# Optimization experiments

Hardware: AMD Instinct MI355X
Metric: run time of the kernel (lower is better)

## Reference

```python
import jax, jax.numpy as jnp
import numpy as np

HID = 256      # cfg.MODEL.YOSO.HIDDEN_DIM
NPROP = 100    # cfg.MODEL.YOSO.NUM_PROPOSALS
K1 = 3         # CONV_KERNEL_SIZE_1D
K2 = 1         # CONV_KERNEL_SIZE_2D
NCLS = 80      # NUM_CLASSES
NHEAD = 8

def layernorm(x, g, b, eps=1e-5):
    m = jnp.mean(x, -1, keepdims=True)
    v = jnp.var(x, -1, keepdims=True)
    return (x - m) * jax.lax.rsqrt(v + eps) * g + b

def dysep(query, value, Wl, bl, ng, nb):
    # dynamic depthwise conv (kernel K1 along feature axis, one kernel per proposal)
    # followed by dynamic pointwise NxN conv, per torch F.conv1d semantics (cross-correlation, 'same' pad)
    w = query @ Wl + bl                      # [B,N,N+K1]
    dw = w[..., :K1]                         # [B,N,K1] depthwise kernels
    pw = w[..., K1:]                         # [B,N,N]  pointwise mixing
    C = value.shape[-1]
    pad = K1 // 2
    vp = jnp.pad(value, ((0, 0), (0, 0), (pad, pad)))
    depth = sum(dw[..., k:k + 1] * vp[..., k:k + C] for k in range(K1))
    depth = jax.nn.relu(depth)
    point = jnp.einsum('bmn,bnc->bmc', pw, depth)
    return layernorm(point, ng, nb)

def mha(x, in_w, in_b, out_w, out_b):
    B, N, E = x.shape
    d = E // NHEAD
    qkv = x @ in_w + in_b
    q, k, v = jnp.split(qkv, 3, axis=-1)
    q = q.reshape(B, N, NHEAD, d)
    k = k.reshape(B, N, NHEAD, d)
    v = v.reshape(B, N, NHEAD, d)
    att = jnp.einsum('bqhd,bkhd->bhqk', q, k) / jnp.sqrt(jnp.asarray(d, x.dtype))
    att = jax.nn.softmax(att, axis=-1)
    o = jnp.einsum('bhqk,bkhd->bqhd', att, v).reshape(B, N, E)
    return o @ out_w + out_b

def setup_inputs() -> dict:
    key = jax.random.key(0)
    ks = iter(jax.random.split(key, 64))
    B, H, W = 8, 128, 128
    E = HID * K2 * K2
    nrm = lambda *s: jax.random.normal(next(ks), s, jnp.float32) * 0.02
    bias_value = -np.log((1 - 0.01) / 0.01)
    return dict(
        features=jax.random.normal(next(ks), (B, HID, H, W), jnp.float32),
        proposal_kernels=jax.random.normal(next(ks), (B, NPROP, E), jnp.float32),
        mask_preds=jax.random.normal(next(ks), (B, NPROP, H, W), jnp.float32),
        fW=nrm(E, NPROP + K1), fb=jnp.zeros(NPROP + K1), fng=jnp.ones(E), fnb=jnp.zeros(E),
        f_norm_g=jnp.ones(E), f_norm_b=jnp.zeros(E),
        kW=nrm(E, NPROP + K1), kb=jnp.zeros(NPROP + K1), kng=jnp.ones(E), knb=jnp.zeros(E),
        k_norm_g=jnp.ones(E), k_norm_b=jnp.zeros(E),
        attn_in_w=nrm(E, 3 * E), attn_in_b=jnp.zeros(3 * E),
        attn_out_w=nrm(E, E), attn_out_b=jnp.zeros(E),
        s_norm_g=jnp.ones(E), s_norm_b=jnp.zeros(E),
        ffn_w1=nrm(HID, 2048), ffn_b1=jnp.zeros(2048),
        ffn_w2=nrm(2048, HID), ffn_b2=jnp.zeros(HID),
        ffn_norm_g=jnp.ones(HID), ffn_norm_b=jnp.zeros(HID),
        cls_w=nrm(HID, HID), cls_ln_g=jnp.ones(HID), cls_ln_b=jnp.zeros(HID),
        fc_cls_w=nrm(HID, NCLS + 1), fc_cls_b=jnp.full((NCLS + 1,), bias_value, jnp.float32),
        mask_w=nrm(3, HID, HID), mask_ln_g=jnp.ones((3, HID)), mask_ln_b=jnp.zeros((3, HID)),
        fc_mask_w=nrm(HID, HID), fc_mask_b=jnp.zeros(HID),
        train_flag=1,
    )

def reference(features, proposal_kernels, mask_preds, fW, fb, fng, fnb, f_norm_g, f_norm_b,
              kW, kb, kng, knb, k_norm_g, k_norm_b,
              attn_in_w, attn_in_b, attn_out_w, attn_out_b, s_norm_g, s_norm_b,
              ffn_w1, ffn_b1, ffn_w2, ffn_b2, ffn_norm_g, ffn_norm_b,
              cls_w, cls_ln_g, cls_ln_b, fc_cls_w, fc_cls_b,
              mask_w, mask_ln_g, mask_ln_b, fc_mask_w, fc_mask_b, train_flag):
    B, C, H, W = features.shape
    hard = (jax.nn.sigmoid(mask_preds) > 0.5).astype(features.dtype)   # hard masks (no grad path)
    f = jnp.einsum('bnhw,bchw->bnc', hard, features)                   # mask-pooled features [B,N,E]
    k = proposal_kernels.reshape(B, NPROP, -1)
    f = layernorm(f + dysep(k, f, fW, fb, fng, fnb), f_norm_g, f_norm_b)
    kk = layernorm(f + dysep(k, f, kW, kb, kng, knb), k_norm_g, k_norm_b)
    kk = layernorm(kk + mha(kk, attn_in_w, attn_in_b, attn_out_w, attn_out_b), s_norm_g, s_norm_b)
    obj = jnp.transpose(kk.reshape(B, NPROP, HID, -1), (0, 1, 3, 2))   # [B,N,K2*K2,HID]
    h = jax.nn.relu(obj @ ffn_w1 + ffn_b1)
    obj = layernorm(obj + (h @ ffn_w2 + ffn_b2), ffn_norm_g, ffn_norm_b)
    cls_feat = obj.sum(-2)                                             # [B,N,HID]
    mask_feat = obj
    if train_flag:
        cls_feat = jax.nn.relu(layernorm(cls_feat @ cls_w, cls_ln_g, cls_ln_b))
        cls_score = (cls_feat @ fc_cls_w + fc_cls_b).reshape(B, NPROP, -1)
    else:
        cls_score = None
    for i in range(mask_w.shape[0]):
        mask_feat = jax.nn.relu(layernorm(mask_feat @ mask_w[i], mask_ln_g[i], mask_ln_b[i]))
    mask_kernels = (mask_feat @ fc_mask_w + fc_mask_b)[:, :, 0, :]     # squeeze(2), K2*K2==1
    new_mask_preds = jnp.einsum('bqc,bchw->bqhw', mask_kernels, features)
    obj_out = jnp.transpose(obj, (0, 1, 3, 2)).reshape(B, NPROP, HID, K2, K2)
    return (cls_score, new_mask_preds, obj_out)
```

## Files before the change

### kernel.cpp

```cpp
#include <hip/hip_runtime.h>

typedef float f32x4 __attribute__((ext_vector_type(4)));
typedef short bfrag __attribute__((ext_vector_type(8)));
typedef short sh4 __attribute__((ext_vector_type(4)));

__device__ __forceinline__ unsigned short f2bf(float x) {
  unsigned int u = __float_as_uint(x);
  return (unsigned short)((u + 0x7FFFu + ((u >> 16) & 1u)) >> 16);
}
__device__ __forceinline__ float bf2f(unsigned short u) {
  return __uint_as_float(((unsigned int)u) << 16);
}
__device__ __forceinline__ float wred_sum(float v) {
#pragma unroll
  for (int o = 32; o > 0; o >>= 1) v += __shfl_xor(v, o);
  return v;
}
__device__ __forceinline__ float wred_max(float v) {
#pragma unroll
  for (int o = 32; o > 0; o >>= 1) v = fmaxf(v, __shfl_xor(v, o));
  return v;
}

struct Prep6 {
  const float* s[6];
  int K[6];
  int N[6];
  int base[6];
  int doff[6];
};

__global__ __launch_bounds__(256) void prep_w(Prep6 p, unsigned short* wt) {
  int t = blockIdx.x;
  int wi = 0;
#pragma unroll
  for (int i = 0; i < 5; ++i)
    if (t >= p.base[i + 1]) wi = i + 1;
  int lt = t - p.base[wi];
  int K = p.K[wi], N = p.N[wi];
  int tkn = (K + 31) >> 5;
  int tk = lt % tkn, tn = lt / tkn;
  __shared__ float tile[32][33];
  const float* src = p.s[wi];
#pragma unroll
  for (int i = 0; i < 4; ++i) {
    int flat = i * 256 + threadIdx.x;
    int kl = flat >> 5, nl = flat & 31;
    int k = tk * 32 + kl, n = tn * 32 + nl;
    tile[kl][nl] = (k < K && n < N) ? src[(size_t)k * N + n] : 0.f;
  }
  __syncthreads();
  unsigned short* dst = wt + p.doff[wi];
#pragma unroll
  for (int i = 0; i < 4; ++i) {
    int flat = i * 256 + threadIdx.x;
    int nl = flat >> 5, kl = flat & 31;
    int k = tk * 32 + kl, n = tn * 32 + nl;
    if (k < K && n < N) {
      int np = (wi < 2) ? ((n >= 3) ? n - 3 : n + 100) : n;
      dst[(size_t)np * K + k] = f2bf(tile[kl][nl]);
    }
  }
}

__global__ __launch_bounds__(256) void prep_bias(const float* __restrict__ fb_,
                                                 const float* __restrict__ kb_,
                                                 float* __restrict__ bfk) {
  int t = threadIdx.x;
  if (t < 103) {
    int np = (t >= 3) ? t - 3 : t + 100;
    bfk[np] = fb_[t];
    bfk[104 + np] = kb_[t];
  }
  if (t == 103) { bfk[103] = 0.f; bfk[207] = 0.f; }
}

struct Cast4 {
  const float* s[4];
  int n[4];
  int base[4];
  int doff[4];
};

__global__ __launch_bounds__(256) void cast_w(Cast4 cc, unsigned short* dst) {
  int t = blockIdx.x;
  int wi = 0;
#pragma unroll
  for (int i = 0; i < 3; ++i)
    if (t >= cc.base[i + 1]) wi = i + 1;
  int lt = t - cc.base[wi];
  int idx = lt * 1024 + threadIdx.x * 4;
  if (idx + 3 < cc.n[wi]) {
    float4 v = *(const float4*)(cc.s[wi] + idx);
    sh4 o;
    o[0] = (short)f2bf(v.x); o[1] = (short)f2bf(v.y);
    o[2] = (short)f2bf(v.z); o[3] = (short)f2bf(v.w);
    *(sh4*)(dst + cc.doff[wi] + idx) = o;
  }
}

__global__ __launch_bounds__(256) void pack_bits(const float* __restrict__ mask,
                                                 unsigned int* __restrict__ bits) {
  int tid = threadIdx.x;
  size_t f = (size_t)blockIdx.x * 256 + tid;
  float4 m = *(const float4*)(mask + f * 4);
  unsigned int n = (m.x > 0.f ? 1u : 0u) | (m.y > 0.f ? 2u : 0u) |
                   (m.z > 0.f ? 4u : 0u) | (m.w > 0.f ? 8u : 0u);
  n <<= ((tid & 7) * 4);
  n |= (unsigned int)__shfl_xor((int)n, 1);
  n |= (unsigned int)__shfl_xor((int)n, 2);
  n |= (unsigned int)__shfl_xor((int)n, 4);
  if ((tid & 7) == 0) bits[((size_t)blockIdx.x * 32) + (tid >> 3)] = n;
}

template <int ABF, int OBF>
__global__ __launch_bounds__(256) void gemm_mf(const void* Av,
                                               const unsigned short* __restrict__ Wt,
                                               const float* __restrict__ bias,
                                               void* Cv, int M, int K, int N, int ldc, int relu,
                                               int kspan) {
  __shared__ short Al[64 * 72];
  __shared__ short Wl[64 * 72];
  int tid = threadIdx.x;
  int r0 = blockIdx.x * 64;
  int c0 = blockIdx.y * 64;
  int kz = blockIdx.z * kspan;
  int w = tid >> 6, lane = tid & 63, quad = lane >> 4, l15 = lane & 15;

  f32x4 acc[4];
#pragma unroll
  for (int mt = 0; mt < 4; ++mt) {
    acc[mt][0] = 0.f; acc[mt][1] = 0.f; acc[mt][2] = 0.f; acc[mt][3] = 0.f;
  }

  for (int k0 = kz; k0 < kz + kspan; k0 += 64) {
    if (ABF) {
      const unsigned short* A = (const unsigned short*)Av;
#pragma unroll
      for (int p = 0; p < 2; ++p) {
        int flat = p * 256 + tid;
        int row = flat >> 3, k8 = flat & 7;
        bfrag v;
        if (r0 + row < M)
          v = *(const bfrag*)(A + (size_t)(r0 + row) * K + k0 + k8 * 8);
        else
          v = (bfrag)(short)0;
        *(bfrag*)(Al + row * 72 + k8 * 8) = v;
      }
    } else {
      const float* A = (const float*)Av;
#pragma unroll
      for (int p = 0; p < 4; ++p) {
        int flat = p * 256 + tid;
        int row = flat >> 4, c4 = flat & 15;
        sh4 o4;
        if (r0 + row < M) {
          float4 v = *(const float4*)(A + (size_t)(r0 + row) * K + k0 + c4 * 4);
          o4[0] = (short)f2bf(v.x); o4[1] = (short)f2bf(v.y);
          o4[2] = (short)f2bf(v.z); o4[3] = (short)f2bf(v.w);
        } else {
          o4[0] = 0; o4[1] = 0; o4[2] = 0; o4[3] = 0;
        }
        *(sh4*)(Al + row * 72 + c4 * 4) = o4;
      }
    }
#pragma unroll
    for (int p = 0; p < 2; ++p) {
      int flat = p * 256 + tid;
      int row = flat >> 3, k8 = flat & 7;
      bfrag v;
      if (c0 + row < N)
        v = *(const bfrag*)(Wt + (size_t)(c0 + row) * K + k0 + k8 * 8);
      else
        v = (bfrag)(short)0;
      *(bfrag*)(Wl + row * 72 + k8 * 8) = v;
    }
    __syncthreads();
#pragma unroll
    for (int kk = 0; kk < 2; ++kk) {
      bfrag bv = *(const bfrag*)(Wl + (w * 16 + l15) * 72 + kk * 32 + quad * 8);
#pragma unroll
      for (int mt = 0; mt < 4; ++mt) {
        bfrag av = *(const bfrag*)(Al + (mt * 16 + l15) * 72 + kk * 32 + quad * 8);
        acc[mt] = __builtin_amdgcn_mfma_f32_16x16x32_bf16(av, bv, acc[mt], 0, 0, 0);
      }
    }
    __syncthreads();
  }
  int col = c0 + w * 16 + l15;
  if (col < N) {
    float bv = bias ? bias[col] : 0.f;
    size_t zoff = (size_t)blockIdx.z * M * ldc;
#pragma unroll
    for (int mt = 0; mt < 4; ++mt)
#pragma unroll
      for (int r = 0; r < 4; ++r) {
        int m = r0 + mt * 16 + quad * 4 + r;
        if (m < M) {
          float v = acc[mt][r] + bv;
          if (relu) v = fmaxf(v, 0.f);
          if (OBF)
            ((unsigned short*)Cv)[zoff + (size_t)m * ldc + col] = f2bf(v);
          else
            ((float*)Cv)[zoff + (size_t)m * ldc + col] = v;
        }
      }
  }
}

__global__ __launch_bounds__(512, 4) void phaseA(const unsigned int* __restrict__ bits,
                                                 const float* __restrict__ feat,
                                                 float* __restrict__ partial) {
  int tid = threadIdx.x;
  int ks = blockIdx.x;
  int ct = blockIdx.y;
  int b  = blockIdx.z;
  __shared__ short Al[2][112 * 72];
  __shared__ short Bl[2][128 * 72];
  int w = tid >> 6, lane = tid & 63, quad = lane >> 4, l15 = lane & 15;

  int rbase = tid >> 4;
  int c4 = tid & 15;
  const float* frow = feat + (size_t)(b * 256 + ct * 128 + rbase) * 16384 + c4 * 4;

  int arow = tid >> 2, q = tid & 3;
  bool aact = tid < 400;
  const unsigned int* brow = bits + (size_t)(b * 100 + arow) * 512 + (q >> 1);

  f32x4 acc[7];
#pragma unroll
  for (int mt = 0; mt < 7; ++mt) {
    acc[mt][0] = 0.f; acc[mt][1] = 0.f; acc[mt][2] = 0.f; acc[mt][3] = 0.f;
  }

  for (int z = tid; z < 384; z += 512) {
    int bufi = z / 192, rem = z % 192;
    sh4 zz; zz[0] = 0; zz[1] = 0; zz[2] = 0; zz[3] = 0;
    *(sh4*)(&Al[bufi][(100 + (rem >> 4)) * 72 + (rem & 15) * 4]) = zz;
  }

  int k0 = ks * 512;
  {
    float4 bpf[4];
    unsigned int awd = 0;
#pragma unroll
    for (int p = 0; p < 4; ++p)
      bpf[p] = *(const float4*)(frow + (size_t)p * 32 * 16384 + k0);
    if (aact) awd = brow[k0 >> 5];
#pragma unroll
    for (int p = 0; p < 4; ++p) {
      int row = rbase + 32 * p;
      sh4 o4b;
      o4b[0] = (short)f2bf(bpf[p].x);
      o4b[1] = (short)f2bf(bpf[p].y);
      o4b[2] = (short)f2bf(bpf[p].z);
      o4b[3] = (short)f2bf(bpf[p].w);
      *(sh4*)(&Bl[0][row * 72 + c4 * 4]) = o4b;
    }
    if (aact) {
      unsigned int hw16 = (awd >> ((q & 1) * 16)) & 0xFFFFu;
      bfrag e0, e1;
#pragma unroll
      for (int i = 0; i < 8; ++i) e0[i] = ((hw16 >> i) & 1u) ? (short)0x3F80 : (short)0;
#pragma unroll
      for (int i = 0; i < 8; ++i) e1[i] = ((hw16 >> (i + 8)) & 1u) ? (short)0x3F80 : (short)0;
      *(bfrag*)(&Al[0][arow * 72 + q * 16]) = e0;
      *(bfrag*)(&Al[0][arow * 72 + q * 16 + 8]) = e1;
    }
  }
  __syncthreads();

  int cur = 0;
  for (int st = 0; st < 8; ++st) {
    float4 bpf[4];
    unsigned int awd = 0;
    if (st < 7) {
      int kb = k0 + (st + 1) * 64;
#pragma unroll
      for (int p = 0; p < 4; ++p)
        bpf[p] = *(const float4*)(frow + (size_t)p * 32 * 16384 + kb);
      if (aact) awd = brow[kb >> 5];
    }
#pragma unroll
    for (int kk = 0; kk < 2; ++kk) {
      bfrag bv = *(const bfrag*)(&Bl[cur][(w * 16 + l15) * 72 + kk * 32 + quad * 8]);
#pragma unroll
      for (int mt = 0; mt < 7; ++mt) {
        bfrag av = *(const bfrag*)(&Al[cur][(mt * 16 + l15) * 72 + kk * 32 + quad * 8]);
        acc[mt] = __builtin_amdgcn_mfma_f32_16x16x32_bf16(av, bv, acc[mt], 0, 0, 0);
      }
    }
    __builtin_amdgcn_sched_barrier(0);
    if (st < 7) {
      int nxt = cur ^ 1;
#pragma unroll
      for (int p = 0; p < 4; ++p) {
        int row = rbase + 32 * p;
        sh4 o4b;
        o4b[0] = (short)f2bf(bpf[p].x);
        o4b[1] = (short)f2bf(bpf[p].y);
        o4b[2] = (short)f2bf(bpf[p].z);
        o4b[3] = (short)f2bf(bpf[p].w);
        *(sh4*)(&Bl[nxt][row * 72 + c4 * 4]) = o4b;
      }
      if (aact) {
        unsigned int hw16 = (awd >> ((q & 1) * 16)) & 0xFFFFu;
        bfrag e0, e1;
#pragma unroll
        for (int i = 0; i < 8; ++i) e0[i] = ((hw16 >> i) & 1u) ? (short)0x3F80 : (short)0;
#pragma unroll
        for (int i = 0; i < 8; ++i) e1[i] = ((hw16 >> (i + 8)) & 1u) ? (short)0x3F80 : (short)0;
        *(bfrag*)(&Al[nxt][arow * 72 + q * 16]) = e0;
        *(bfrag*)(&Al[nxt][arow * 72 + q * 16 + 8]) = e1;
      }
    }
    __syncthreads();
    cur ^= 1;
  }

  float* pb = partial + (size_t)(b * 32 + ks) * (100 * 256) + ct * 128 + w * 16 + l15;
#pragma unroll
  for (int mt = 0; mt < 7; ++mt)
#pragma unroll
    for (int r = 0; r < 4; ++r) {
      int m = mt * 16 + quad * 4 + r;
      if (m < 100) pb[(size_t)m * 256] = acc[mt][r];
    }
}

__global__ __launch_bounds__(256) void reduceA(const float* __restrict__ partial,
                                               float* __restrict__ fm) {
  int gid = blockIdx.x * 256 + threadIdx.x;
  int c = gid & 255, row = gid >> 8;
  int b = row / 100, n = row % 100;
  float s = 0.f;
#pragma unroll
  for (int ks = 0; ks < 32; ++ks)
    s += partial[((size_t)(b * 32 + ks) * 100 + n) * 256 + c];
  fm[(size_t)row * 256 + c] = s;
}

__global__ __launch_bounds__(256) void pointdw(const float* __restrict__ fm,
                                               const float* __restrict__ wbuf,
                                               float* __restrict__ point) {
  int tid = threadIdx.x;
  int b = blockIdx.y, c0 = blockIdx.x * 32;
  __shared__ float dl[100 * 33];
  for (int flat = tid; flat < 3200; flat += 256) {
    int n = flat >> 5, cl = flat & 31, c = c0 + cl;
    const float* fr = fm + (size_t)(b * 100 + n) * 256;
    const float* wr = wbuf + (size_t)(b * 100 + n) * 208;
    float x0 = (c > 0) ? fr[c - 1] : 0.f;
    float x1 = fr[c];
    float x2 = (c < 255) ? fr[c + 1] : 0.f;
    float d = wr[100] * x0 + wr[101] * x1 + wr[102] * x2;
    dl[n * 33 + cl] = fmaxf(d, 0.f);
  }
  __syncthreads();
  int cl = tid & 31, mg = tid >> 5;
  for (int m = mg; m < 100; m += 8) {
    const float4* pw4 = (const float4*)(wbuf + (size_t)(b * 100 + m) * 208);
    float a = 0.f;
#pragma unroll
    for (int n4 = 0; n4 < 25; ++n4) {
      float4 wv = pw4[n4];
      a += wv.x * dl[(n4 * 4 + 0) * 33 + cl] + wv.y * dl[(n4 * 4 + 1) * 33 + cl]
         + wv.z * dl[(n4 * 4 + 2) * 33 + cl] + wv.w * dl[(n4 * 4 + 3) * 33 + cl];
    }
    point[(size_t)(b * 100 + m) * 256 + c0 + cl] = a;
  }
}

__global__ __launch_bounds__(256) void ln2_kernel(const float* __restrict__ x,
                                                  const float* __restrict__ resid,
                                                  const float* __restrict__ g1, const float* __restrict__ b1,
                                                  const float* __restrict__ g2, const float* __restrict__ b2,
                                                  float* __restrict__ out) {
  int tid = threadIdx.x;
  int row = blockIdx.x * 4 + (tid >> 6);
  int lane = tid & 63;
  size_t base = (size_t)row * 256 + lane * 4;
  float4 v = *(const float4*)(x + base);
  float mean = wred_sum(v.x + v.y + v.z + v.w) * (1.f / 256.f);
  float d0 = v.x - mean, d1 = v.y - mean, d2 = v.z - mean, d3 = v.w - mean;
  float rs = rsqrtf(wred_sum(d0 * d0 + d1 * d1 + d2 * d2 + d3 * d3) * (1.f / 256.f) + 1e-5f);
  float4 gv = *(const float4*)(g1 + lane * 4);
  float4 bv = *(const float4*)(b1 + lane * 4);
  float4 rv = *(const float4*)(resid + base);
  float y0 = rv.x + d0 * rs * gv.x + bv.x;
  float y1 = rv.y + d1 * rs * gv.y + bv.y;
  float y2 = rv.z + d2 * rs * gv.z + bv.z;
  float y3 = rv.w + d3 * rs * gv.w + bv.w;
  float mean2 = wred_sum(y0 + y1 + y2 + y3) * (1.f / 256.f);
  float e0 = y0 - mean2, e1 = y1 - mean2, e2 = y2 - mean2, e3 = y3 - mean2;
  float rs2 = rsqrtf(wred_sum(e0 * e0 + e1 * e1 + e2 * e2 + e3 * e3) * (1.f / 256.f) + 1e-5f);
  float4 g2v = *(const float4*)(g2 + lane * 4);
  float4 b2v = *(const float4*)(b2 + lane * 4);
  float4 o;
  o.x = e0 * rs2 * g2v.x + b2v.x;
  o.y = e1 * rs2 * g2v.y + b2v.y;
  o.z = e2 * rs2 * g2v.z + b2v.z;
  o.w = e3 * rs2 * g2v.w + b2v.w;
  *(float4*)(out + base) = o;
}

__global__ __launch_bounds__(256) void ln_kernel(const float* __restrict__ x,
                                                 const float* __restrict__ res,
                                                 const float* __restrict__ g, const float* __restrict__ bb,
                                                 float* __restrict__ out, int relu,
                                                 float* __restrict__ copy2) {
  int tid = threadIdx.x;
  int row = blockIdx.x * 4 + (tid >> 6);
  int lane = tid & 63;
  size_t base = (size_t)row * 256 + lane * 4;
  float4 v = *(const float4*)(x + base);
  if (res) {
    float4 rv = *(const float4*)(res + base);
    v.x += rv.x; v.y += rv.y; v.z += rv.z; v.w += rv.w;
  }
  float mean = wred_sum(v.x + v.y + v.z + v.w) * (1.f / 256.f);
  float d0 = v.x - mean, d1 = v.y - mean, d2 = v.z - mean, d3 = v.w - mean;
  float rs = rsqrtf(wred_sum(d0 * d0 + d1 * d1 + d2 * d2 + d3 * d3) * (1.f / 256.f) + 1e-5f);
  float4 gv = *(const float4*)(g + lane * 4);
  float4 bv = *(const float4*)(bb + lane * 4);
  float4 o;
  o.x = d0 * rs * gv.x + bv.x;
  o.y = d1 * rs * gv.y + bv.y;
  o.z = d2 * rs * gv.z + bv.z;
  o.w = d3 * rs * gv.w + bv.w;
  if (relu) {
    o.x = fmaxf(o.x, 0.f); o.y = fmaxf(o.y, 0.f);
    o.z = fmaxf(o.z, 0.f); o.w = fmaxf(o.w, 0.f);
  }
  *(float4*)(out + base) = o;
  if (copy2) *(float4*)(copy2 + base) = o;
}

__global__ __launch_bounds__(256) void ln_ffn2(const float* __restrict__ t1,
                                               const float* __restrict__ b2,
                                               const float* __restrict__ res,
                                               const float* __restrict__ g, const float* __restrict__ bb,
                                               float* __restrict__ out,
                                               float* __restrict__ copy2) {
  int tid = threadIdx.x;
  int row = blockIdx.x * 4 + (tid >> 6);
  int lane = tid & 63;
  size_t base = (size_t)row * 256 + lane * 4;
  float4 v = *(const float4*)(t1 + base);
#pragma unroll
  for (int s = 1; s < 4; ++s) {
    float4 p = *(const float4*)(t1 + (size_t)s * 204800 + base);
    v.x += p.x; v.y += p.y; v.z += p.z; v.w += p.w;
  }
  float4 b2v = *(const float4*)(b2 + lane * 4);
  float4 rv = *(const float4*)(res + base);
  v.x += b2v.x + rv.x; v.y += b2v.y + rv.y; v.z += b2v.z + rv.z; v.w += b2v.w + rv.w;
  float mean = wred_sum(v.x + v.y + v.z + v.w) * (1.f / 256.f);
  float d0 = v.x - mean, d1 = v.y - mean, d2 = v.z - mean, d3 = v.w - mean;
  float rs = rsqrtf(wred_sum(d0 * d0 + d1 * d1 + d2 * d2 + d3 * d3) * (1.f / 256.f) + 1e-5f);
  float4 gv = *(const float4*)(g + lane * 4);
  float4 bv = *(const float4*)(bb + lane * 4);
  float4 o;
  o.x = d0 * rs * gv.x + bv.x;
  o.y = d1 * rs * gv.y + bv.y;
  o.z = d2 * rs * gv.z + bv.z;
  o.w = d3 * rs * gv.w + bv.w;
  *(float4*)(out + base) = o;
  *(float4*)(copy2 + base) = o;
}

__global__ __launch_bounds__(256) void attn_kernel(const float* __restrict__ qkv,
                                                   float* __restrict__ obuf) {
  int tid = threadIdx.x;
  int b = blockIdx.y, h = blockIdx.x & 7, qq = blockIdx.x >> 3;
  __shared__ float ktj[100 * 32];
  __shared__ unsigned short vl[100 * 32];
  __shared__ float sl[25 * 100];
  const float* base = qkv + (size_t)b * 100 * 768;
  for (int flat = tid; flat < 3200; flat += 256) {
    int j = flat >> 5, dd = flat & 31;
    ktj[j * 32 + dd] = base[(size_t)j * 768 + 256 + h * 32 + dd];
    vl[j * 32 + dd] = f2bf(base[(size_t)j * 768 + 512 + h * 32 + dd]);
  }
  __syncthreads();
  {
    int il = tid % 25;
    int jseg = tid / 25;
    int i = qq * 25 + il;
    const float4* q4 = (const float4*)(base + (size_t)i * 768 + h * 32);
    float4 q[8];
#pragma unroll
    for (int d4 = 0; d4 < 8; ++d4) q[d4] = q4[d4];
    if (jseg < 10) {
      for (int jj = 0; jj < 10; ++jj) {
        int j = jseg * 10 + jj;
        const float4* kr = (const float4*)(ktj + j * 32);
        float a = 0.f;
#pragma unroll
        for (int d4 = 0; d4 < 8; ++d4) {
          float4 kv = kr[d4];
          a += q[d4].x * kv.x + q[d4].y * kv.y + q[d4].z * kv.z + q[d4].w * kv.w;
        }
        sl[il * 100 + j] = a * 0.17677669529663687f;
      }
    }
  }
  __syncthreads();
  int w = tid >> 6, lane = tid & 63;
  for (int r = w; r < 25; r += 4) {
    float x0 = sl[r * 100 + lane];
    float x1 = (lane + 64 < 100) ? sl[r * 100 + lane + 64] : -1e30f;
    float mx = wred_max(fmaxf(x0, x1));
    float e0 = __expf(x0 - mx);
    float e1 = (lane + 64 < 100) ? __expf(x1 - mx) : 0.f;
    float inv = 1.f / wred_sum(e0 + e1);
    sl[r * 100 + lane] = e0 * inv;
    if (lane + 64 < 100) sl[r * 100 + lane + 64] = e1 * inv;
  }
  __syncthreads();
  for (int flat = tid; flat < 800; flat += 256) {
    int il = flat >> 5, dd = flat & 31;
    float a = 0.f;
#pragma unroll 4
    for (int j = 0; j < 100; ++j) a += sl[il * 100 + j] * bf2f(vl[j * 32 + dd]);
    obuf[(size_t)(b * 100 + qq * 25 + il) * 256 + h * 32 + dd] = a;
  }
}

__global__ __launch_bounds__(256) void head_fused(
    const float* __restrict__ objb,
    const unsigned short* __restrict__ whd,
    const float* __restrict__ cls_g, const float* __restrict__ cls_b,
    const float* __restrict__ fcclsb,
    const float* __restrict__ mask_g, const float* __restrict__ mask_b,
    const float* __restrict__ fcmb,
    float* __restrict__ out_cls, unsigned short* __restrict__ mk16) {
  const int WH_CLS = 0, WH_FCCLS = 65536, WH_M = 86272, WH_FCM = 282880;
  int tid = threadIdx.x, wv = tid >> 6, lane = tid & 63;
  int row = blockIdx.x;
  __shared__ float xs[256];
  __shared__ float x0s[256];
  __shared__ float ps[4][256];
  if (wv == 0) {
    float4 v = *(const float4*)(objb + (size_t)row * 256 + lane * 4);
    *(float4*)(&xs[lane * 4]) = v;
    *(float4*)(&x0s[lane * 4]) = v;
  }
  __syncthreads();
  int c = lane * 4;
  int kb = wv * 64;

  for (int li = 0; li < 3; ++li) {
    const unsigned short* W = whd + WH_M + li * 65536;
    float a0 = 0.f, a1 = 0.f, a2 = 0.f, a3 = 0.f;
#pragma unroll 8
    for (int k = kb; k < kb + 64; ++k) {
      float xk = xs[k];
      sh4 w4 = *(const sh4*)(W + (size_t)k * 256 + c);
      a0 += xk * bf2f((unsigned short)w4[0]);
      a1 += xk * bf2f((unsigned short)w4[1]);
      a2 += xk * bf2f((unsigned short)w4[2]);
      a3 += xk * bf2f((unsigned short)w4[3]);
    }
    ps[wv][c] = a0; ps[wv][c + 1] = a1; ps[wv][c + 2] = a2; ps[wv][c + 3] = a3;
    __syncthreads();
    float s0 = ps[0][c] + ps[1][c] + ps[2][c] + ps[3][c];
    float s1 = ps[0][c + 1] + ps[1][c + 1] + ps[2][c + 1] + ps[3][c + 1];
    float s2 = ps[0][c + 2] + ps[1][c + 2] + ps[2][c + 2] + ps[3][c + 2];
    float s3 = ps[0][c + 3] + ps[1][c + 3] + ps[2][c + 3] + ps[3][c + 3];
    float mean = wred_sum(s0 + s1 + s2 + s3) * (1.f / 256.f);
    float d0 = s0 - mean, d1 = s1 - mean, d2 = s2 - mean, d3 = s3 - mean;
    float rs = rsqrtf(wred_sum(d0 * d0 + d1 * d1 + d2 * d2 + d3 * d3) * (1.f / 256.f) + 1e-5f);
    float4 gv = *(const float4*)(mask_g + li * 256 + c);
    float4 bv = *(const float4*)(mask_b + li * 256 + c);
    float4 o;
    o.x = fmaxf(d0 * rs * gv.x + bv.x, 0.f);
    o.y = fmaxf(d1 * rs * gv.y + bv.y, 0.f);
    o.z = fmaxf(d2 * rs * gv.z + bv.z, 0.f);
    o.w = fmaxf(d3 * rs * gv.w + bv.w, 0.f);
    __syncthreads();
    *(float4*)(&xs[c]) = o;
    __syncthreads();
  }
  {
    const unsigned short* W = whd + WH_FCM;
    float a0 = 0.f, a1 = 0.f, a2 = 0.f, a3 = 0.f;
#pragma unroll 8
    for (int k = kb; k < kb + 64; ++k) {
      float xk = xs[k];
      sh4 w4 = *(const sh4*)(W + (size_t)k * 256 + c);
      a0 += xk * bf2f((unsigned short)w4[0]);
      a1 += xk * bf2f((unsigned short)w4[1]);
      a2 += xk * bf2f((unsigned short)w4[2]);
      a3 += xk * bf2f((unsigned short)w4[3]);
    }
    ps[wv][c] = a0; ps[wv][c + 1] = a1; ps[wv][c + 2] = a2; ps[wv][c + 3] = a3;
    __syncthreads();
    if (wv == 0) {
      float s0 = ps[0][c] + ps[1][c] + ps[2][c] + ps[3][c];
      float s1 = ps[0][c + 1] + ps[1][c + 1] + ps[2][c + 1] + ps[3][c + 1];
      float s2 = ps[0][c + 2] + ps[1][c + 2] + ps[2][c + 2] + ps[3][c + 2];
      float s3 = ps[0][c + 3] + ps[1][c + 3] + ps[2][c + 3] + ps[3][c + 3];
      float4 bv = *(const float4*)(fcmb + c);
      sh4 o;
      o[0] = (short)f2bf(s0 + bv.x); o[1] = (short)f2bf(s1 + bv.y);
      o[2] = (short)f2bf(s2 + bv.z); o[3] = (short)f2bf(s3 + bv.w);
      *(sh4*)(mk16 + (size_t)row * 256 + c) = o;
    }
    __syncthreads();
  }
  {
    const unsigned short* W = whd + WH_CLS;
    float a0 = 0.f, a1 = 0.f, a2 = 0.f, a3 = 0.f;
#pragma unroll 8
    for (int k = kb; k < kb + 64; ++k) {
      float xk = x0s[k];
      sh4 w4 = *(const sh4*)(W + (size_t)k * 256 + c);
      a0 += xk * bf2f((unsigned short)w4[0]);
      a1 += xk * bf2f((unsigned short)w4[1]);
      a2 += xk * bf2f((unsigned short)w4[2]);
      a3 += xk * bf2f((unsigned short)w4[3]);
    }
    ps[wv][c] = a0; ps[wv][c + 1] = a1; ps[wv][c + 2] = a2; ps[wv][c + 3] = a3;
    __syncthreads();
    float s0 = ps[0][c] + ps[1][c] + ps[2][c] + ps[3][c];
    float s1 = ps[0][c + 1] + ps[1][c + 1] + ps[2][c + 1] + ps[3][c + 1];
    float s2 = ps[0][c + 2] + ps[1][c + 2] + ps[2][c + 2] + ps[3][c + 2];
    float s3 = ps[0][c + 3] + ps[1][c + 3] + ps[2][c + 3] + ps[3][c + 3];
    float mean = wred_sum(s0 + s1 + s2 + s3) * (1.f / 256.f);
    float d0 = s0 - mean, d1 = s1 - mean, d2 = s2 - mean, d3 = s3 - mean;
    float rs = rsqrtf(wred_sum(d0 * d0 + d1 * d1 + d2 * d2 + d3 * d3) * (1.f / 256.f) + 1e-5f);
    float4 gv = *(const float4*)(cls_g + c);
    float4 bv = *(const float4*)(cls_b + c);
    float4 o;
    o.x = fmaxf(d0 * rs * gv.x + bv.x, 0.f);
    o.y = fmaxf(d1 * rs * gv.y + bv.y, 0.f);
    o.z = fmaxf(d2 * rs * gv.z + bv.z, 0.f);
    o.w = fmaxf(d3 * rs * gv.w + bv.w, 0.f);
    __syncthreads();
    *(float4*)(&xs[c]) = o;
    __syncthreads();
  }
  {
    const unsigned short* W = whd + WH_FCCLS;
    float a0 = 0.f, a1 = 0.f;
#pragma unroll 8
    for (int k = kb; k < kb + 64; ++k) {
      float xk = xs[k];
      a0 += xk * bf2f(W[(size_t)k * 81 + lane]);
      if (lane < 17) a1 += xk * bf2f(W[(size_t)k * 81 + 64 + lane]);
    }
    ps[wv][lane] = a0;
    if (lane < 17) ps[wv][64 + lane] = a1;
    __syncthreads();
    if (wv == 0) {
      float s = ps[0][lane] + ps[1][lane] + ps[2][lane] + ps[3][lane];
      out_cls[(size_t)row * 81 + lane] = s + fcclsb[lane];
      if (lane < 17) {
        float s2 = ps[0][64 + lane] + ps[1][64 + lane] + ps[2][64 + lane] + ps[3][64 + lane];
        out_cls[(size_t)row * 81 + 64 + lane] = s2 + fcclsb[64 + lane];
      }
    }
  }
}

__global__ __launch_bounds__(256, 4) void phaseE(const unsigned short* __restrict__ mk16,
                                                 const float* __restrict__ feat,
                                                 float* __restrict__ out) {
  int tid = threadIdx.x;
  int b = blockIdx.y;
  int hw0 = blockIdx.x * 128;
  int w = tid >> 6, lane = tid & 63, quad = lane >> 4, l15 = lane & 15;
  f32x4 acc[7][2];
#pragma unroll
  for (int mt = 0; mt < 7; ++mt)
#pragma unroll
    for (int nt = 0; nt < 2; ++nt) {
      acc[mt][nt][0] = 0.f; acc[mt][nt][1] = 0.f; acc[mt][nt][2] = 0.f; acc[mt][nt][3] = 0.f;
    }
  size_t fb = (size_t)b * 256 * 16384;
  int hwl = hw0 + w * 32 + l15;
  const unsigned short* mkb_b = mk16 + (size_t)b * 100 * 256;
  for (int kk = 0; kk < 8; ++kk) {
    bfrag bv[2];
#pragma unroll
    for (int nt = 0; nt < 2; ++nt) {
#pragma unroll
      for (int j = 0; j < 8; ++j) {
        float v = feat[fb + (size_t)(kk * 32 + quad * 8 + j) * 16384 + hwl + nt * 16];
        bv[nt][j] = (short)f2bf(v);
      }
    }
    bfrag av[7];
#pragma unroll
    for (int mt = 0; mt < 7; ++mt) {
      int row = mt * 16 + l15;
      int rr = (row < 100) ? row : 0;
      av[mt] = *(const bfrag*)(mkb_b + (size_t)rr * 256 + kk * 32 + quad * 8);
    }
#pragma unroll
    for (int mt = 0; mt < 7; ++mt) {
      acc[mt][0] = __builtin_amdgcn_mfma_f32_16x16x32_bf16(av[mt], bv[0], acc[mt][0], 0, 0, 0);
      acc[mt][1] = __builtin_amdgcn_mfma_f32_16x16x32_bf16(av[mt], bv[1], acc[mt][1], 0, 0, 0);
    }
  }
#pragma unroll
  for (int mt = 0; mt < 7; ++mt)
#pragma unroll
    for (int nt = 0; nt < 2; ++nt)
#pragma unroll
      for (int r = 0; r < 4; ++r) {
        int m = mt * 16 + quad * 4 + r;
        if (m < 100)
          out[(size_t)(b * 100 + m) * 16384 + hw0 + w * 32 + nt * 16 + l15] = acc[mt][nt][r];
      }
}

extern "C" void kernel_launch(void* const* d_in, const int* in_sizes, int n_in,
                              void* d_out, int out_size, void* d_ws, size_t ws_size,
                              hipStream_t stream) {
  const float* feat    = (const float*)d_in[0];
  const float* prop    = (const float*)d_in[1];
  const float* maskp   = (const float*)d_in[2];
  const float* fW      = (const float*)d_in[3];
  const float* fb_     = (const float*)d_in[4];
  const float* fng     = (const float*)d_in[5];
  const float* fnb     = (const float*)d_in[6];
  const float* f_ng    = (const float*)d_in[7];
  const float* f_nb    = (const float*)d_in[8];
  const float* kW      = (const float*)d_in[9];
  const float* kb_     = (const float*)d_in[10];
  const float* kng     = (const float*)d_in[11];
  const float* knb     = (const float*)d_in[12];
  const float* k_ng    = (const float*)d_in[13];
  const float* k_nb    = (const float*)d_in[14];
  const float* aw_in   = (const float*)d_in[15];
  const float* ab_in   = (const float*)d_in[16];
  const float* aw_out  = (const float*)d_in[17];
  const float* ab_out  = (const float*)d_in[18];
  const float* s_ng    = (const float*)d_in[19];
  const float* s_nb    = (const float*)d_in[20];
  const float* w1      = (const float*)d_in[21];
  const float* b1      = (const float*)d_in[22];
  const float* w2      = (const float*)d_in[23];
  const float* b2      = (const float*)d_in[24];
  const float* ffn_ng  = (const float*)d_in[25];
  const float* ffn_nb  = (const float*)d_in[26];
  const float* cls_w   = (const float*)d_in[27];
  const float* cls_g   = (const float*)d_in[28];
  const float* cls_b   = (const float*)d_in[29];
  const float* fcclsw  = (const float*)d_in[30];
  const float* fcclsb  = (const float*)d_in[31];
  const float* mask_w  = (const float*)d_in[32];
  const float* mask_g  = (const float*)d_in[33];
  const float* mask_b  = (const float*)d_in[34];
  const float* fcmw    = (const float*)d_in[35];
  const float* fcmb    = (const float*)d_in[36];
  float* out = (float*)d_out;

  float* ws = (float*)d_ws;
  size_t off = 0;
  unsigned short* wt = (unsigned short*)(ws + off); off += 681984;
  float* fm      = ws + off; off += 204800;
  float* bias_fk = ws + off; off += 208;
  unsigned int* bitsbuf = (unsigned int*)(ws + off); off += 409600;
  unsigned short* whd = (unsigned short*)(ws + off); off += 174208;
  float* partial = ws + off;
  float* ub = partial;
  size_t uo = 0;
  float* wb   = ub + uo; uo += 166400;
  float* pt   = ub + uo; uo += 204800;
  float* fbuf = ub + uo; uo += 204800;
  float* kkb  = ub + uo; uo += 204800;
  float* qkvb = ub + uo; uo += 614400;
  float* ob   = ub + uo; uo += 204800;
  float* mo   = ub + uo; uo += 204800;
  float* kk2  = ub + uo; uo += 204800;
  float* t1   = ub + uo; uo += 819200;
  float* objb = ub + uo; uo += 204800;
  float* mkb  = ub + uo; uo += 204800;
  unsigned short* ffn1b = (unsigned short*)(ub + uo); uo += 409600;
  unsigned short* mkb16 = (unsigned short*)mkb;

  const int wt_fW = 0, wt_kW = 26624, wt_ain = 53248, wt_aout = 249856;
  const int wt_w1 = 315392, wt_w2 = 839680;

  float* out_cls  = out;
  float* out_mask = out + 64800;
  float* out_obj  = out + 64800 + 13107200;

  Prep6 p;
  const float* srcs[6] = {fW, kW, aw_in, aw_out, w1, w2};
  int Ks[6]    = {256, 256, 256, 256, 256, 2048};
  int Ns[6]    = {103, 103, 768, 256, 2048, 256};
  int doffs[6] = {wt_fW, wt_kW, wt_ain, wt_aout, wt_w1, wt_w2};
  int tb = 0;
  for (int i = 0; i < 6; ++i) {
    p.s[i] = srcs[i]; p.K[i] = Ks[i]; p.N[i] = Ns[i]; p.doff[i] = doffs[i];
    p.base[i] = tb;
    tb += ((Ks[i] + 31) / 32) * ((Ns[i] + 31) / 32);
  }
  prep_w<<<tb, 256, 0, stream>>>(p, wt);
  prep_bias<<<1, 256, 0, stream>>>(fb_, kb_, bias_fk);
  Cast4 cc;
  const float* csrc[4] = {cls_w, fcclsw, mask_w, fcmw};
  int cn[4] = {65536, 20736, 196608, 65536};
  int cdoff[4] = {0, 65536, 86272, 282880};
  int cb = 0;
  for (int i = 0; i < 4; ++i) {
    cc.s[i] = csrc[i]; cc.n[i] = cn[i]; cc.doff[i] = cdoff[i];
    cc.base[i] = cb;
    cb += (cn[i] + 1023) / 1024;
  }
  cast_w<<<cb, 256, 0, stream>>>(cc, whd);
  pack_bits<<<12800, 256, 0, stream>>>(maskp, bitsbuf);

  phaseA<<<dim3(32, 2, 8), 512, 0, stream>>>(bitsbuf, feat, partial);
  reduceA<<<800, 256, 0, stream>>>(partial, fm);
  gemm_mf<0, 0><<<dim3(13, 4, 1), 256, 0, stream>>>(prop, wt + wt_fW, bias_fk, wb, 800, 256, 208, 208, 0, 256);
  pointdw<<<dim3(8, 8), 256, 0, stream>>>(fm, wb, pt);
  ln2_kernel<<<200, 256, 0, stream>>>(pt, fm, fng, fnb, f_ng, f_nb, fbuf);
  pointdw<<<dim3(8, 8), 256, 0, stream>>>(fbuf, wb + 104, pt);
  ln2_kernel<<<200, 256, 0, stream>>>(pt, fbuf, kng, knb, k_ng, k_nb, kkb);
  gemm_mf<0, 0><<<dim3(13, 12, 1), 256, 0, stream>>>(kkb, wt + wt_ain, ab_in, qkvb, 800, 256, 768, 768, 0, 256);
  attn_kernel<<<dim3(32, 8), 256, 0, stream>>>(qkvb, ob);
  gemm_mf<0, 0><<<dim3(13, 4, 1), 256, 0, stream>>>(ob, wt + wt_aout, ab_out, mo, 800, 256, 256, 256, 0, 256);
  ln_kernel<<<200, 256, 0, stream>>>(mo, kkb, s_ng, s_nb, kk2, 0, nullptr);
  gemm_mf<0, 1><<<dim3(13, 32, 1), 256, 0, stream>>>(kk2, wt + wt_w1, b1, ffn1b, 800, 256, 2048, 2048, 1, 256);
  gemm_mf<1, 0><<<dim3(13, 4, 4), 256, 0, stream>>>(ffn1b, wt + wt_w2, nullptr, t1, 800, 2048, 256, 256, 0, 512);
  ln_ffn2<<<200, 256, 0, stream>>>(t1, b2, kk2, ffn_ng, ffn_nb, objb, out_obj);
  head_fused<<<800, 256, 0, stream>>>(objb, whd, cls_g, cls_b, fcclsb,
                                      mask_g, mask_b, fcmb, out_cls, mkb16);
  phaseE<<<dim3(128, 8), 256, 0, stream>>>(mkb16, feat, out_mask);
}
```

Before: 588.0 us.

## Shrink phaseA channel tile to 64 and drop double buffering; widen pointdw grid

phaseA now uses 256-thread blocks covering 64 feature channels instead of 512 threads over 128. It drops the LDS double buffer in favour of a single-buffered load, sync, compute loop, and the grid doubles in channel tiles. The goal is more blocks and higher occupancy from smaller LDS use, since the kernel is bound by streaming the features. The cost is no overlap between global loads and MFMA within a block, with the mask-bit A tile rebuilt per block and twice as many blocks doing it. pointdw also halves its channel tile to 16 to launch twice as many blocks.

```diff
diff --git a/kernel.cpp b/kernel.cpp
--- a/kernel.cpp
+++ b/kernel.cpp
@@ -208,24 +208,23 @@
   }
 }
 
-__global__ __launch_bounds__(512, 4) void phaseA(const unsigned int* __restrict__ bits,
+__global__ __launch_bounds__(256, 6) void phaseA(const unsigned int* __restrict__ bits,
                                                  const float* __restrict__ feat,
                                                  float* __restrict__ partial) {
   int tid = threadIdx.x;
   int ks = blockIdx.x;
   int ct = blockIdx.y;
   int b  = blockIdx.z;
-  __shared__ short Al[2][112 * 72];
-  __shared__ short Bl[2][128 * 72];
+  __shared__ short Al[112 * 72];
+  __shared__ short Bl[64 * 72];
   int w = tid >> 6, lane = tid & 63, quad = lane >> 4, l15 = lane & 15;
 
-  int rbase = tid >> 4;
-  int c4 = tid & 15;
-  const float* frow = feat + (size_t)(b * 256 + ct * 128 + rbase) * 16384 + c4 * 4;
-
-  int arow = tid >> 2, q = tid & 3;
-  bool aact = tid < 400;
-  const unsigned int* brow = bits + (size_t)(b * 100 + arow) * 512 + (q >> 1);
+  int brow = tid >> 2, s = tid & 3;
+  const float* frow = feat + (size_t)(b * 256 + ct * 64 + brow) * 16384 + s * 4;
+
+  int arow = tid >> 1, half = tid & 1;
+  bool aact = tid < 200;
+  const unsigned int* browb = bits + (size_t)(b * 100 + arow) * 512 + half;
 
   f32x4 acc[7];
 #pragma unroll
@@ -233,92 +232,52 @@
     acc[mt][0] = 0.f; acc[mt][1] = 0.f; acc[mt][2] = 0.f; acc[mt][3] = 0.f;
   }
 
-  for (int z = tid; z < 384; z += 512) {
-    int bufi = z / 192, rem = z % 192;
+  for (int z = tid; z < 216; z += 256) {
     sh4 zz; zz[0] = 0; zz[1] = 0; zz[2] = 0; zz[3] = 0;
-    *(sh4*)(&Al[bufi][(100 + (rem >> 4)) * 72 + (rem & 15) * 4]) = zz;
+    *(sh4*)(&Al[(100 + z / 18) * 72 + (z % 18) * 4]) = zz;
   }
 
   int k0 = ks * 512;
-  {
+  for (int st = 0; st < 8; ++st) {
+    int kb = k0 + st * 64;
     float4 bpf[4];
-    unsigned int awd = 0;
-#pragma unroll
-    for (int p = 0; p < 4; ++p)
-      bpf[p] = *(const float4*)(frow + (size_t)p * 32 * 16384 + k0);
-    if (aact) awd = brow[k0 >> 5];
-#pragma unroll
-    for (int p = 0; p < 4; ++p) {
-      int row = rbase + 32 * p;
-      sh4 o4b;
-      o4b[0] = (short)f2bf(bpf[p].x);
-      o4b[1] = (short)f2bf(bpf[p].y);
-      o4b[2] = (short)f2bf(bpf[p].z);
-      o4b[3] = (short)f2bf(bpf[p].w);
-      *(sh4*)(&Bl[0][row * 72 + c4 * 4]) = o4b;
+#pragma unroll
+    for (int i = 0; i < 4; ++i)
+      bpf[i] = *(const float4*)(frow + kb + i * 16);
+    unsigned int awd = aact ? browb[kb >> 5] : 0u;
+    __syncthreads();
+#pragma unroll
+    for (int i = 0; i < 4; ++i) {
+      sh4 o4;
+      o4[0] = (short)f2bf(bpf[i].x);
+      o4[1] = (short)f2bf(bpf[i].y);
+      o4[2] = (short)f2bf(bpf[i].z);
+      o4[3] = (short)f2bf(bpf[i].w);
+      *(sh4*)(&Bl[brow * 72 + i * 16 + s * 4]) = o4;
     }
     if (aact) {
-      unsigned int hw16 = (awd >> ((q & 1) * 16)) & 0xFFFFu;
-      bfrag e0, e1;
-#pragma unroll
-      for (int i = 0; i < 8; ++i) e0[i] = ((hw16 >> i) & 1u) ? (short)0x3F80 : (short)0;
-#pragma unroll
-      for (int i = 0; i < 8; ++i) e1[i] = ((hw16 >> (i + 8)) & 1u) ? (short)0x3F80 : (short)0;
-      *(bfrag*)(&Al[0][arow * 72 + q * 16]) = e0;
-      *(bfrag*)(&Al[0][arow * 72 + q * 16 + 8]) = e1;
-    }
-  }
-  __syncthreads();
-
-  int cur = 0;
-  for (int st = 0; st < 8; ++st) {
-    float4 bpf[4];
-    unsigned int awd = 0;
-    if (st < 7) {
-      int kb = k0 + (st + 1) * 64;
-#pragma unroll
-      for (int p = 0; p < 4; ++p)
-        bpf[p] = *(const float4*)(frow + (size_t)p * 32 * 16384 + kb);
-      if (aact) awd = brow[kb >> 5];
-    }
+#pragma unroll
+      for (int j = 0; j < 4; ++j) {
+        bfrag e;
+#pragma unroll
+        for (int i2 = 0; i2 < 8; ++i2)
+          e[i2] = ((awd >> (j * 8 + i2)) & 1u) ? (short)0x3F80 : (short)0;
+        *(bfrag*)(&Al[arow * 72 + half * 32 + j * 8]) = e;
+      }
+    }
+    __syncthreads();
 #pragma unroll
     for (int kk = 0; kk < 2; ++kk) {
-      bfrag bv = *(const bfrag*)(&Bl[cur][(w * 16 + l15) * 72 + kk * 32 + quad * 8]);
+      bfrag bv = *(const bfrag*)(&Bl[(w * 16 + l15) * 72 + kk * 32 + quad * 8]);
 #pragma unroll
       for (int mt = 0; mt < 7; ++mt) {
-        bfrag av = *(const bfrag*)(&Al[cur][(mt * 16 + l15) * 72 + kk * 32 + quad * 8]);
+        bfrag av = *(const bfrag*)(&Al[(mt * 16 + l15) * 72 + kk * 32 + quad * 8]);
         acc[mt] = __builtin_amdgcn_mfma_f32_16x16x32_bf16(av, bv, acc[mt], 0, 0, 0);
       }
     }
-    __builtin_amdgcn_sched_barrier(0);
-    if (st < 7) {
-      int nxt = cur ^ 1;
-#pragma unroll
-      for (int p = 0; p < 4; ++p) {
-        int row = rbase + 32 * p;
-        sh4 o4b;
-        o4b[0] = (short)f2bf(bpf[p].x);
-        o4b[1] = (short)f2bf(bpf[p].y);
-        o4b[2] = (short)f2bf(bpf[p].z);
-        o4b[3] = (short)f2bf(bpf[p].w);
-        *(sh4*)(&Bl[nxt][row * 72 + c4 * 4]) = o4b;
-      }
-      if (aact) {
-        unsigned int hw16 = (awd >> ((q & 1) * 16)) & 0xFFFFu;
-        bfrag e0, e1;
-#pragma unroll
-        for (int i = 0; i < 8; ++i) e0[i] = ((hw16 >> i) & 1u) ? (short)0x3F80 : (short)0;
-#pragma unroll
-        for (int i = 0; i < 8; ++i) e1[i] = ((hw16 >> (i + 8)) & 1u) ? (short)0x3F80 : (short)0;
-        *(bfrag*)(&Al[nxt][arow * 72 + q * 16]) = e0;
-        *(bfrag*)(&Al[nxt][arow * 72 + q * 16 + 8]) = e1;
-      }
-    }
-    __syncthreads();
-    cur ^= 1;
-  }
-
-  float* pb = partial + (size_t)(b * 32 + ks) * (100 * 256) + ct * 128 + w * 16 + l15;
+  }
+
+  float* pb = partial + (size_t)(b * 32 + ks) * (100 * 256) + ct * 64 + w * 16 + l15;
 #pragma unroll
   for (int mt = 0; mt < 7; ++mt)
 #pragma unroll
@@ -344,28 +303,28 @@
                                                const float* __restrict__ wbuf,
                                                float* __restrict__ point) {
   int tid = threadIdx.x;
-  int b = blockIdx.y, c0 = blockIdx.x * 32;
-  __shared__ float dl[100 * 33];
-  for (int flat = tid; flat < 3200; flat += 256) {
-    int n = flat >> 5, cl = flat & 31, c = c0 + cl;
+  int b = blockIdx.y, c0 = blockIdx.x * 16;
+  __shared__ float dl[100 * 17];
+  for (int flat = tid; flat < 1600; flat += 256) {
+    int n = flat >> 4, cl = flat & 15, c = c0 + cl;
     const float* fr = fm + (size_t)(b * 100 + n) * 256;
     const float* wr = wbuf + (size_t)(b * 100 + n) * 208;
     float x0 = (c > 0) ? fr[c - 1] : 0.f;
     float x1 = fr[c];
     float x2 = (c < 255) ? fr[c + 1] : 0.f;
     float d = wr[100] * x0 + wr[101] * x1 + wr[102] * x2;
-    dl[n * 33 + cl] = fmaxf(d, 0.f);
+    dl[n * 17 + cl] = fmaxf(d, 0.f);
   }
   __syncthreads();
-  int cl = tid & 31, mg = tid >> 5;
-  for (int m = mg; m < 100; m += 8) {
+  int cl = tid & 15, mg = tid >> 4;
+  for (int m = mg; m < 100; m += 16) {
     const float4* pw4 = (const float4*)(wbuf + (size_t)(b * 100 + m) * 208);
     float a = 0.f;
 #pragma unroll
     for (int n4 = 0; n4 < 25; ++n4) {
       float4 wv = pw4[n4];
-      a += wv.x * dl[(n4 * 4 + 0) * 33 + cl] + wv.y * dl[(n4 * 4 + 1) * 33 + cl]
-         + wv.z * dl[(n4 * 4 + 2) * 33 + cl] + wv.w * dl[(n4 * 4 + 3) * 33 + cl];
+      a += wv.x * dl[(n4 * 4 + 0) * 17 + cl] + wv.y * dl[(n4 * 4 + 1) * 17 + cl]
+         + wv.z * dl[(n4 * 4 + 2) * 17 + cl] + wv.w * dl[(n4 * 4 + 3) * 17 + cl];
     }
     point[(size_t)(b * 100 + m) * 256 + c0 + cl] = a;
   }
@@ -815,12 +774,12 @@
   cast_w<<<cb, 256, 0, stream>>>(cc, whd);
   pack_bits<<<12800, 256, 0, stream>>>(maskp, bitsbuf);
 
-  phaseA<<<dim3(32, 2, 8), 512, 0, stream>>>(bitsbuf, feat, partial);
+  phaseA<<<dim3(32, 4, 8), 256, 0, stream>>>(bitsbuf, feat, partial);
   reduceA<<<800, 256, 0, stream>>>(partial, fm);
   gemm_mf<0, 0><<<dim3(13, 4, 1), 256, 0, stream>>>(prop, wt + wt_fW, bias_fk, wb, 800, 256, 208, 208, 0, 256);
-  pointdw<<<dim3(8, 8), 256, 0, stream>>>(fm, wb, pt);
+  pointdw<<<dim3(16, 8), 256, 0, stream>>>(fm, wb, pt);
   ln2_kernel<<<200, 256, 0, stream>>>(pt, fm, fng, fnb, f_ng, f_nb, fbuf);
-  pointdw<<<dim3(8, 8), 256, 0, stream>>>(fbuf, wb + 104, pt);
+  pointdw<<<dim3(16, 8), 256, 0, stream>>>(fbuf, wb + 104, pt);
   ln2_kernel<<<200, 256, 0, stream>>>(pt, fbuf, kng, knb, k_ng, k_nb, kkb);
   gemm_mf<0, 0><<<dim3(13, 12, 1), 256, 0, stream>>>(kkb, wt + wt_ain, ab_in, qkvb, 800, 256, 768, 768, 0, 256);
   attn_kernel<<<dim3(32, 8), 256, 0, stream>>>(qkvb, ob);
```

Result: faster. 556.8 us (-5.3%).
